# Performance work log

Measured on AMD Instinct MI355X. Metric: run time of the kernel, lower is better.

The kernel has to match this reference:

```python
import jax, jax.numpy as jnp
import numpy as np

B, S, D, H = 2, 2048, 1024, 16
HD = D // H  # head dim = 64

def setup_inputs() -> dict:
    key = jax.random.key(0)
    ks = jax.random.split(key, 3)
    scale = 1.0 / np.sqrt(D)
    return {
        "x": jax.random.normal(ks[0], (B, S, D), jnp.float32),
        "W_attn": jax.random.normal(ks[1], (D, 3 * D), jnp.float32) * scale,
        "b_attn": jnp.zeros((3 * D,), jnp.float32),
        "W_proj": jax.random.normal(ks[2], (D, D), jnp.float32) * scale,
        "b_proj": jnp.zeros((D,), jnp.float32),
    }

def reference(x, W_attn, b_attn, W_proj, b_proj):
    b, s, d = x.shape
    qkv = x @ W_attn + b_attn                      # [B,S,3D]
    q, k, v = jnp.split(qkv, 3, axis=-1)
    # [B,S,D] -> [B,H,S,HD]
    def heads(t):
        return t.reshape(b, s, H, HD).transpose(0, 2, 1, 3)
    q, k, v = heads(q), heads(k), heads(v)
    scores = jnp.einsum('bhqd,bhkd->bhqk', q, k) * (1.0 / np.sqrt(HD))
    causal = jnp.tril(jnp.ones((s, s), dtype=bool))
    scores = jnp.where(causal[None, None], scores, -jnp.inf)
    probs = jax.nn.softmax(scores, axis=-1)
    y = jnp.einsum('bhqk,bhkd->bhqd', probs, v)    # [B,H,S,HD]
    y = y.transpose(0, 2, 1, 3).reshape(b, s, d)
    return y @ W_proj + b_proj
```

## Files before the change

### kernel.cpp

```cpp
#include <hip/hip_runtime.h>

typedef __bf16 bf16;
typedef __bf16 bf16x4 __attribute__((ext_vector_type(4)));
typedef __bf16 bf16x8 __attribute__((ext_vector_type(8)));
typedef float f32x4 __attribute__((ext_vector_type(4)));

#define S_LEN 2048
#define D_DIM 1024
#define N_HEAD 16
#define HEAD_DIM 64
#define M_TOK 4096
#define BH 32

#define EXP2F(x) __builtin_amdgcn_exp2f(x)
#define Q_SCALE 0.18033688f

#define SW(r, c) ((c) ^ (((r) & 3) << 4))

typedef __attribute__((address_space(3))) void lds_void;
typedef const __attribute__((address_space(1))) void gbl_void;

__device__ __forceinline__ void gl_lds16(const bf16* g, bf16* l) {
  __builtin_amdgcn_global_load_lds((gbl_void*)g, (lds_void*)l, 16, 0, 0);
}

__global__ __launch_bounds__(256) void k_cast(const float* __restrict__ x,
                                              bf16* __restrict__ o, int n) {
  int i = (blockIdx.x * 256 + threadIdx.x) * 4;
  if (i >= n) return;
  float4 v = *(const float4*)(x + i);
  bf16x4 w;
  w[0] = (bf16)v.x; w[1] = (bf16)v.y; w[2] = (bf16)v.z; w[3] = (bf16)v.w;
  *(bf16x4*)(o + i) = w;
}

__global__ __launch_bounds__(256) void k_transpose(const float* __restrict__ W,
                                                   bf16* __restrict__ Wt,
                                                   int K, int N) {
  __shared__ float tile[32][33];
  int nb = blockIdx.x, kb = blockIdx.y;
  int t = threadIdx.x;
  int r = t >> 3, c4 = (t & 7) * 4;
  float4 v = *(const float4*)&W[(kb * 32 + r) * N + nb * 32 + c4];
  tile[r][c4 + 0] = v.x; tile[r][c4 + 1] = v.y;
  tile[r][c4 + 2] = v.z; tile[r][c4 + 3] = v.w;
  __syncthreads();
  bf16x4 o;
  #pragma unroll
  for (int i = 0; i < 4; i++) o[i] = (bf16)tile[c4 + i][r];
  *(bf16x4*)&Wt[(nb * 32 + r) * K + kb * 32 + c4] = o;
}

__global__ __launch_bounds__(256, 2)
void k_gemm_qkv(const bf16* __restrict__ A, const bf16* __restrict__ Bt,
                const float* __restrict__ bias,
                bf16* __restrict__ qk, bf16* __restrict__ vT) {
  __shared__ bf16 As[128 * 32];
  __shared__ bf16 Bs[128 * 32];
  const int K = 1024;
  int bn = blockIdx.x, bm = blockIdx.y;
  int t = threadIdx.x;
  int wave = t >> 6, lane = t & 63, c = lane & 15, quad = lane >> 4;
  int wm = wave & 1, wn = wave >> 1;
  int ldrow = lane >> 2, ldcol = (lane & 3) * 8;

  const bf16* Ag = A + (size_t)(bm * 128) * K;
  const bf16* Bg = Bt + (size_t)(bn * 128) * K;

  f32x4 acc[4][4] = {};

  for (int k0 = 0; k0 < K; k0 += 32) {
    __syncthreads();
    #pragma unroll
    for (int q = 0; q < 2; q++) {
      int r0 = (wave * 2 + q) * 16;
      gl_lds16(&Ag[(size_t)(r0 + ldrow) * K + k0 + ldcol], &As[r0 * 32]);
      gl_lds16(&Bg[(size_t)(r0 + ldrow) * K + k0 + ldcol], &Bs[r0 * 32]);
    }
    __syncthreads();
    bf16x8 af[4];
    #pragma unroll
    for (int mt = 0; mt < 4; mt++)
      af[mt] = *(const bf16x8*)&As[(wm * 64 + mt * 16 + c) * 32 + quad * 8];
    #pragma unroll
    for (int nt = 0; nt < 4; nt++) {
      bf16x8 bfr = *(const bf16x8*)&Bs[(wn * 64 + nt * 16 + c) * 32 + quad * 8];
      #pragma unroll
      for (int mt = 0; mt < 4; mt++)
        acc[mt][nt] = __builtin_amdgcn_mfma_f32_16x16x32_bf16(af[mt], bfr, acc[mt][nt], 0, 0, 0);
    }
  }

  #pragma unroll
  for (int nt = 0; nt < 4; nt++) {
    int n = bn * 128 + wn * 64 + nt * 16 + c;
    int which = n >> 10, nl = n & 1023;
    int h = nl >> 6, hd = nl & 63;
    float bv = bias[n];
    #pragma unroll
    for (int mt = 0; mt < 4; mt++) {
      int m0 = bm * 128 + wm * 64 + mt * 16 + quad * 4;
      int b = m0 >> 11, s0 = m0 & 2047;
      int bh = b * N_HEAD + h;
      if (which == 2) {
        bf16x4 o;
        #pragma unroll
        for (int r = 0; r < 4; r++) o[r] = (bf16)(acc[mt][nt][r] + bv);
        *(bf16x4*)&vT[((size_t)bh * HEAD_DIM + hd) * S_LEN + s0] = o;
      } else if (which == 0) {
        #pragma unroll
        for (int r = 0; r < 4; r++)
          qk[(bh * S_LEN + s0 + r) * HEAD_DIM + hd] = (bf16)((acc[mt][nt][r] + bv) * Q_SCALE);
      } else {
        #pragma unroll
        for (int r = 0; r < 4; r++)
          qk[BH * S_LEN * HEAD_DIM + (bh * S_LEN + s0 + r) * HEAD_DIM + hd] = (bf16)(acc[mt][nt][r] + bv);
      }
    }
  }
}

__global__ __launch_bounds__(256, 2)
void k_attn(const bf16* __restrict__ qk, const bf16* __restrict__ vT,
            bf16* __restrict__ y) {
  __shared__ bf16 Ks[2][64][64];
  __shared__ bf16 Vs[2][64][64];
  __shared__ bf16 Ps[128][64];
  int bx = blockIdx.x;
  int bh = bx & 31;
  int p = bx >> 5;
  int t = threadIdx.x, w = t >> 6, lane = t & 63, c = lane & 15, quad = lane >> 4;
  const bf16* Qg = qk + (size_t)bh * (S_LEN * HEAD_DIM);
  const bf16* Kg = qk + (size_t)(BH + bh) * (S_LEN * HEAD_DIM);
  const bf16* Vg = vT + (size_t)bh * (HEAD_DIM * S_LEN);
  int b = bh >> 4, h = bh & 15;
  int srow = t >> 3, scol = (t & 7) * 8;
  int swcol = SW(srow, scol);

  const int tileQ0 = p, tileQ1 = 31 - p;
  const int nkb = 32 - p;
  const int dthr = w * 16 + c;

  bf16x8 qf[2][2];
  f32x4 acc[2][4] = {};
  float mM[2] = {-1e30f, -1e30f}, lL[2] = {0.f, 0.f};
  {
    int qr0 = tileQ0 * 64 + w * 16 + c;
    int qr1 = tileQ1 * 64 + w * 16 + c;
    qf[0][0] = *(const bf16x8*)&Qg[qr0 * HEAD_DIM + quad * 8];
    qf[0][1] = *(const bf16x8*)&Qg[qr0 * HEAD_DIM + 32 + quad * 8];
    qf[1][0] = *(const bf16x8*)&Qg[qr1 * HEAD_DIM + quad * 8];
    qf[1][1] = *(const bf16x8*)&Qg[qr1 * HEAD_DIM + 32 + quad * 8];
  }

  bf16x8 kr0 = *(const bf16x8*)&Kg[srow * HEAD_DIM + scol];
  bf16x8 kr1 = *(const bf16x8*)&Kg[(srow + 32) * HEAD_DIM + scol];
  bf16x8 vr0 = *(const bf16x8*)&Vg[(size_t)srow * S_LEN + scol];
  bf16x8 vr1 = *(const bf16x8*)&Vg[(size_t)(srow + 32) * S_LEN + scol];
  *(bf16x8*)&Ks[0][srow][swcol] = kr0;
  *(bf16x8*)&Ks[0][srow + 32][swcol] = kr1;
  *(bf16x8*)&Vs[0][srow][swcol] = vr0;
  *(bf16x8*)&Vs[0][srow + 32][swcol] = vr1;

  for (int kb = 0; kb < nkb; kb++) {
    __syncthreads();
    int cur = kb & 1;
    bool haveNext = (kb + 1 < nkb);
    if (haveNext) {
      kr0 = *(const bf16x8*)&Kg[((kb + 1) * 64 + srow) * HEAD_DIM + scol];
      kr1 = *(const bf16x8*)&Kg[((kb + 1) * 64 + srow + 32) * HEAD_DIM + scol];
      vr0 = *(const bf16x8*)&Vg[(size_t)srow * S_LEN + (kb + 1) * 64 + scol];
      vr1 = *(const bf16x8*)&Vg[(size_t)(srow + 32) * S_LEN + (kb + 1) * 64 + scol];
    }

    bool act0 = (kb <= p);
    bool dia0 = (kb == p);
    bool dia1 = (kb == 31 - p);

    f32x4 sc[2][4];
    #pragma unroll
    for (int kt = 0; kt < 4; kt++) {
      int kr = kt * 16 + c;
      bf16x8 kf0 = *(const bf16x8*)&Ks[cur][kr][SW(kr, quad * 8)];
      bf16x8 kf1 = *(const bf16x8*)&Ks[cur][kr][SW(kr, 32 + quad * 8)];
      if (act0) {
        f32x4 z = {};
        z = __builtin_amdgcn_mfma_f32_16x16x32_bf16(kf0, qf[0][0], z, 0, 0, 0);
        z = __builtin_amdgcn_mfma_f32_16x16x32_bf16(kf1, qf[0][1], z, 0, 0, 0);
        sc[0][kt] = z;
      }
      f32x4 z = {};
      z = __builtin_amdgcn_mfma_f32_16x16x32_bf16(kf0, qf[1][0], z, 0, 0, 0);
      z = __builtin_amdgcn_mfma_f32_16x16x32_bf16(kf1, qf[1][1], z, 0, 0, 0);
      sc[1][kt] = z;
    }

    if (dia0) {
      #pragma unroll
      for (int kt = 0; kt < 4; kt++)
        #pragma unroll
        for (int r = 0; r < 4; r++)
          if (kt * 16 + quad * 4 + r > dthr) sc[0][kt][r] = -1e30f;
    }
    if (dia1) {
      #pragma unroll
      for (int kt = 0; kt < 4; kt++)
        #pragma unroll
        for (int r = 0; r < 4; r++)
          if (kt * 16 + quad * 4 + r > dthr) sc[1][kt][r] = -1e30f;
    }

    #pragma unroll
    for (int st = 0; st < 2; st++) {
      if (st == 0 && !act0) continue;
      float mx = sc[st][0][0];
      #pragma unroll
      for (int kt = 0; kt < 4; kt++)
        #pragma unroll
        for (int r = 0; r < 4; r++) mx = fmaxf(mx, sc[st][kt][r]);
      mx = fmaxf(mx, __shfl_xor(mx, 16));
      mx = fmaxf(mx, __shfl_xor(mx, 32));
      float mnew = fmaxf(mM[st], mx);
      float alpha = EXP2F(mM[st] - mnew);
      float sum = 0.f;
      int prow = st * 64 + w * 16 + c;
      #pragma unroll
      for (int kt = 0; kt < 4; kt++) {
        bf16x4 pk;
        #pragma unroll
        for (int r = 0; r < 4; r++) {
          float pv = EXP2F(sc[st][kt][r] - mnew);
          sum += pv;
          pk[r] = (bf16)pv;
        }
        *(bf16x4*)&Ps[prow][SW(prow, kt * 16 + quad * 4)] = pk;
      }
      sum += __shfl_xor(sum, 16);
      sum += __shfl_xor(sum, 32);
      lL[st] = lL[st] * alpha + sum;
      mM[st] = mnew;
      #pragma unroll
      for (int dt = 0; dt < 4; dt++)
        #pragma unroll
        for (int r = 0; r < 4; r++) acc[st][dt][r] *= alpha;
    }

    #pragma unroll
    for (int ks = 0; ks < 2; ks++) {
      int prow1 = 64 + w * 16 + c;
      bf16x8 pf1 = *(const bf16x8*)&Ps[prow1][SW(prow1, ks * 32 + quad * 8)];
      bf16x8 pf0;
      if (act0) {
        int prow0 = w * 16 + c;
        pf0 = *(const bf16x8*)&Ps[prow0][SW(prow0, ks * 32 + quad * 8)];
      }
      #pragma unroll
      for (int dt = 0; dt < 4; dt++) {
        int vrow = dt * 16 + c;
        bf16x8 vf = *(const bf16x8*)&Vs[cur][vrow][SW(vrow, ks * 32 + quad * 8)];
        if (act0)
          acc[0][dt] = __builtin_amdgcn_mfma_f32_16x16x32_bf16(vf, pf0, acc[0][dt], 0, 0, 0);
        acc[1][dt] = __builtin_amdgcn_mfma_f32_16x16x32_bf16(vf, pf1, acc[1][dt], 0, 0, 0);
      }
    }

    if (haveNext) {
      int nxt = cur ^ 1;
      *(bf16x8*)&Ks[nxt][srow][swcol] = kr0;
      *(bf16x8*)&Ks[nxt][srow + 32][swcol] = kr1;
      *(bf16x8*)&Vs[nxt][srow][swcol] = vr0;
      *(bf16x8*)&Vs[nxt][srow + 32][swcol] = vr1;
    }
  }

  #pragma unroll
  for (int st = 0; st < 2; st++) {
    int q = (st == 0 ? tileQ0 : tileQ1) * 64 + w * 16 + c;
    float linv = 1.0f / lL[st];
    #pragma unroll
    for (int dt = 0; dt < 4; dt++) {
      bf16x4 o;
      #pragma unroll
      for (int r = 0; r < 4; r++) o[r] = (bf16)(acc[st][dt][r] * linv);
      *(bf16x4*)&y[((size_t)(b * S_LEN + q) * N_HEAD + h) * HEAD_DIM + dt * 16 + quad * 4] = o;
    }
  }
}

__global__ __launch_bounds__(256, 2)
void k_gemm_proj(const bf16* __restrict__ A, const bf16* __restrict__ Bt,
                 const float* __restrict__ bias, float* __restrict__ out) {
  __shared__ bf16 As[128 * 32];
  __shared__ bf16 Bs[64 * 32];
  const int K = 1024;
  int bn = blockIdx.x, bm = blockIdx.y;
  int t = threadIdx.x;
  int wave = t >> 6, lane = t & 63, c = lane & 15, quad = lane >> 4;
  int wm = wave & 1, wn = wave >> 1;
  int ldrow = lane >> 2, ldcol = (lane & 3) * 8;

  const bf16* Ag = A + (size_t)(bm * 128) * K;
  const bf16* Bg = Bt + (size_t)(bn * 64) * K;

  f32x4 acc[4][2] = {};

  for (int k0 = 0; k0 < K; k0 += 32) {
    __syncthreads();
    #pragma unroll
    for (int q = 0; q < 2; q++) {
      int r0 = (wave * 2 + q) * 16;
      gl_lds16(&Ag[(size_t)(r0 + ldrow) * K + k0 + ldcol], &As[r0 * 32]);
    }
    gl_lds16(&Bg[(size_t)(wave * 16 + ldrow) * K + k0 + ldcol], &Bs[wave * 16 * 32]);
    __syncthreads();
    bf16x8 af[4];
    #pragma unroll
    for (int mt = 0; mt < 4; mt++)
      af[mt] = *(const bf16x8*)&As[(wm * 64 + mt * 16 + c) * 32 + quad * 8];
    #pragma unroll
    for (int nt = 0; nt < 2; nt++) {
      bf16x8 bfr = *(const bf16x8*)&Bs[(wn * 32 + nt * 16 + c) * 32 + quad * 8];
      #pragma unroll
      for (int mt = 0; mt < 4; mt++)
        acc[mt][nt] = __builtin_amdgcn_mfma_f32_16x16x32_bf16(af[mt], bfr, acc[mt][nt], 0, 0, 0);
    }
  }

  #pragma unroll
  for (int nt = 0; nt < 2; nt++) {
    int n = bn * 64 + wn * 32 + nt * 16 + c;
    float bv = bias[n];
    #pragma unroll
    for (int mt = 0; mt < 4; mt++) {
      #pragma unroll
      for (int r = 0; r < 4; r++) {
        int m = bm * 128 + wm * 64 + mt * 16 + quad * 4 + r;
        out[(size_t)m * D_DIM + n] = acc[mt][nt][r] + bv;
      }
    }
  }
}

extern "C" void kernel_launch(void* const* d_in, const int* in_sizes, int n_in,
                              void* d_out, int out_size, void* d_ws, size_t ws_size,
                              hipStream_t stream) {
  const float* x      = (const float*)d_in[0];
  const float* W_attn = (const float*)d_in[1];
  const float* b_attn = (const float*)d_in[2];
  const float* W_proj = (const float*)d_in[3];
  const float* b_proj = (const float*)d_in[4];
  float* out = (float*)d_out;

  bf16* x_bf = (bf16*)d_ws;
  bf16* wat  = x_bf + 4096 * 1024;
  bf16* wpt  = wat + 3072 * 1024;
  bf16* qk   = wpt + 1024 * 1024;
  bf16* vT   = qk + 8 * 1024 * 1024;
  bf16* y_bf = vT + 4 * 1024 * 1024;

  k_cast<<<4096, 256, 0, stream>>>(x, x_bf, 4096 * 1024);
  k_transpose<<<dim3(3072 / 32, 1024 / 32), 256, 0, stream>>>(W_attn, wat, 1024, 3072);
  k_transpose<<<dim3(1024 / 32, 1024 / 32), 256, 0, stream>>>(W_proj, wpt, 1024, 1024);
  k_gemm_qkv<<<dim3(24, 32), 256, 0, stream>>>(x_bf, wat, b_attn, qk, vT);
  k_attn<<<512, 256, 0, stream>>>(qk, vT, y_bf);
  k_gemm_proj<<<dim3(16, 32), 256, 0, stream>>>(y_bf, wpt, b_proj, out);
}
```

Measured before the change: 190.7 us.

## Split paired causal Q tiles into one tile per block, heaviest-first ordering

Measured after the change: 186.5 us. 2.2% less time.

```diff
diff --git a/kernel.cpp b/kernel.cpp
--- a/kernel.cpp
+++ b/kernel.cpp
@@ -120,15 +120,15 @@
   }
 }
 
-__global__ __launch_bounds__(256, 2)
+__global__ __launch_bounds__(256, 4)
 void k_attn(const bf16* __restrict__ qk, const bf16* __restrict__ vT,
             bf16* __restrict__ y) {
   __shared__ bf16 Ks[2][64][64];
   __shared__ bf16 Vs[2][64][64];
-  __shared__ bf16 Ps[128][64];
+  __shared__ bf16 Ps[64][64];
   int bx = blockIdx.x;
   int bh = bx & 31;
-  int p = bx >> 5;
+  int tile = 31 - (bx >> 5);
   int t = threadIdx.x, w = t >> 6, lane = t & 63, c = lane & 15, quad = lane >> 4;
   const bf16* Qg = qk + (size_t)bh * (S_LEN * HEAD_DIM);
   const bf16* Kg = qk + (size_t)(BH + bh) * (S_LEN * HEAD_DIM);
@@ -137,20 +137,16 @@
   int srow = t >> 3, scol = (t & 7) * 8;
   int swcol = SW(srow, scol);
 
-  const int tileQ0 = p, tileQ1 = 31 - p;
-  const int nkb = 32 - p;
+  const int nkb = tile + 1;
   const int dthr = w * 16 + c;
 
-  bf16x8 qf[2][2];
-  f32x4 acc[2][4] = {};
-  float mM[2] = {-1e30f, -1e30f}, lL[2] = {0.f, 0.f};
+  bf16x8 qf[2];
+  f32x4 acc[4] = {};
+  float mM = -1e30f, lL = 0.f;
   {
-    int qr0 = tileQ0 * 64 + w * 16 + c;
-    int qr1 = tileQ1 * 64 + w * 16 + c;
-    qf[0][0] = *(const bf16x8*)&Qg[qr0 * HEAD_DIM + quad * 8];
-    qf[0][1] = *(const bf16x8*)&Qg[qr0 * HEAD_DIM + 32 + quad * 8];
-    qf[1][0] = *(const bf16x8*)&Qg[qr1 * HEAD_DIM + quad * 8];
-    qf[1][1] = *(const bf16x8*)&Qg[qr1 * HEAD_DIM + 32 + quad * 8];
+    int qr = tile * 64 + w * 16 + c;
+    qf[0] = *(const bf16x8*)&Qg[qr * HEAD_DIM + quad * 8];
+    qf[1] = *(const bf16x8*)&Qg[qr * HEAD_DIM + 32 + quad * 8];
   }
 
   bf16x8 kr0 = *(const bf16x8*)&Kg[srow * HEAD_DIM + scol];
@@ -173,63 +169,46 @@
       vr1 = *(const bf16x8*)&Vg[(size_t)(srow + 32) * S_LEN + (kb + 1) * 64 + scol];
     }
 
-    bool act0 = (kb <= p);
-    bool dia0 = (kb == p);
-    bool dia1 = (kb == 31 - p);
-
-    f32x4 sc[2][4];
+    bool dia = (kb == tile);
+
+    f32x4 sc[4];
     #pragma unroll
     for (int kt = 0; kt < 4; kt++) {
       int kr = kt * 16 + c;
       bf16x8 kf0 = *(const bf16x8*)&Ks[cur][kr][SW(kr, quad * 8)];
       bf16x8 kf1 = *(const bf16x8*)&Ks[cur][kr][SW(kr, 32 + quad * 8)];
-      if (act0) {
-        f32x4 z = {};
-        z = __builtin_amdgcn_mfma_f32_16x16x32_bf16(kf0, qf[0][0], z, 0, 0, 0);
-        z = __builtin_amdgcn_mfma_f32_16x16x32_bf16(kf1, qf[0][1], z, 0, 0, 0);
-        sc[0][kt] = z;
-      }
       f32x4 z = {};
-      z = __builtin_amdgcn_mfma_f32_16x16x32_bf16(kf0, qf[1][0], z, 0, 0, 0);
-      z = __builtin_amdgcn_mfma_f32_16x16x32_bf16(kf1, qf[1][1], z, 0, 0, 0);
-      sc[1][kt] = z;
-    }
-
-    if (dia0) {
+      z = __builtin_amdgcn_mfma_f32_16x16x32_bf16(kf0, qf[0], z, 0, 0, 0);
+      z = __builtin_amdgcn_mfma_f32_16x16x32_bf16(kf1, qf[1], z, 0, 0, 0);
+      sc[kt] = z;
+    }
+
+    if (dia) {
       #pragma unroll
       for (int kt = 0; kt < 4; kt++)
         #pragma unroll
         for (int r = 0; r < 4; r++)
-          if (kt * 16 + quad * 4 + r > dthr) sc[0][kt][r] = -1e30f;
-    }
-    if (dia1) {
+          if (kt * 16 + quad * 4 + r > dthr) sc[kt][r] = -1e30f;
+    }
+
+    {
+      float mx = sc[0][0];
       #pragma unroll
       for (int kt = 0; kt < 4; kt++)
         #pragma unroll
-        for (int r = 0; r < 4; r++)
-          if (kt * 16 + quad * 4 + r > dthr) sc[1][kt][r] = -1e30f;
-    }
-
-    #pragma unroll
-    for (int st = 0; st < 2; st++) {
-      if (st == 0 && !act0) continue;
-      float mx = sc[st][0][0];
-      #pragma unroll
-      for (int kt = 0; kt < 4; kt++)
-        #pragma unroll
-        for (int r = 0; r < 4; r++) mx = fmaxf(mx, sc[st][kt][r]);
+        for (int r = 0; r < 4; r++) mx = fmaxf(mx, sc[kt][r]);
       mx = fmaxf(mx, __shfl_xor(mx, 16));
       mx = fmaxf(mx, __shfl_xor(mx, 32));
-      float mnew = fmaxf(mM[st], mx);
-      float alpha = EXP2F(mM[st] - mnew);
+      float mnew = fmaxf(mM, mx);
+      float alpha = EXP2F(mM - mnew);
       float sum = 0.f;
-      int prow = st * 64 + w * 16 + c;
+      int prow = w * 16 + c;
       #pragma unroll
       for (int kt = 0; kt < 4; kt++) {
         bf16x4 pk;
         #pragma unroll
         for (int r = 0; r < 4; r++) {
-          float pv = EXP2F(sc[st][kt][r] - mnew);
+          float pv = EXP2F(sc[kt][r] - mnew);
           sum += pv;
           pk[r] = (bf16)pv;
         }
@@ -237,30 +216,25 @@
       }
       sum += __shfl_xor(sum, 16);
       sum += __shfl_xor(sum, 32);
-      lL[st] = lL[st] * alpha + sum;
-      mM[st] = mnew;
+      lL = lL * alpha + sum;
+      mM = mnew;
       #pragma unroll
       for (int dt = 0; dt < 4; dt++)
         #pragma unroll
-        for (int r = 0; r < 4; r++) acc[st][dt][r] *= alpha;
-    }
-
-    #pragma unroll
-    for (int ks = 0; ks < 2; ks++) {
-      int prow1 = 64 + w * 16 + c;
-      bf16x8 pf1 = *(const bf16x8*)&Ps[prow1][SW(prow1, ks * 32 + quad * 8)];
-      bf16x8 pf0;
-      if (act0) {
-        int prow0 = w * 16 + c;
-        pf0 = *(const bf16x8*)&Ps[prow0][SW(prow0, ks * 32 + quad * 8)];
-      }
-      #pragma unroll
-      for (int dt = 0; dt < 4; dt++) {
-        int vrow = dt * 16 + c;
-        bf16x8 vf = *(const bf16x8*)&Vs[cur][vrow][SW(vrow, ks * 32 + quad * 8)];
-        if (act0)
-          acc[0][dt] = __builtin_amdgcn_mfma_f32_16x16x32_bf16(vf, pf0, acc[0][dt], 0, 0, 0);
-        acc[1][dt] = __builtin_amdgcn_mfma_f32_16x16x32_bf16(vf, pf1, acc[1][dt], 0, 0, 0);
+        for (int r = 0; r < 4; r++) acc[dt][r] *= alpha;
+    }
+
+    {
+      int prow = w * 16 + c;
+      #pragma unroll
+      for (int ks = 0; ks < 2; ks++) {
+        bf16x8 pf = *(const bf16x8*)&Ps[prow][SW(prow, ks * 32 + quad * 8)];
+        #pragma unroll
+        for (int dt = 0; dt < 4; dt++) {
+          int vrow = dt * 16 + c;
+          bf16x8 vf = *(const bf16x8*)&Vs[cur][vrow][SW(vrow, ks * 32 + quad * 8)];
+          acc[dt] = __builtin_amdgcn_mfma_f32_16x16x32_bf16(vf, pf, acc[dt], 0, 0, 0);
+        }
       }
     }
 
@@ -273,15 +247,14 @@
     }
   }
 
-  #pragma unroll
-  for (int st = 0; st < 2; st++) {
-    int q = (st == 0 ? tileQ0 : tileQ1) * 64 + w * 16 + c;
-    float linv = 1.0f / lL[st];
+  {
+    int q = tile * 64 + w * 16 + c;
+    float linv = 1.0f / lL;
     #pragma unroll
     for (int dt = 0; dt < 4; dt++) {
       bf16x4 o;
       #pragma unroll
-      for (int r = 0; r < 4; r++) o[r] = (bf16)(acc[st][dt][r] * linv);
+      for (int r = 0; r < 4; r++) o[r] = (bf16)(acc[dt][r] * linv);
       *(bf16x4*)&y[((size_t)(b * S_LEN + q) * N_HEAD + h) * HEAD_DIM + dt * 16 + quad * 4] = o;
     }
   }
@@ -362,6 +335,6 @@
   k_transpose<<<dim3(3072 / 32, 1024 / 32), 256, 0, stream>>>(W_attn, wat, 1024, 3072);
   k_transpose<<<dim3(1024 / 32, 1024 / 32), 256, 0, stream>>>(W_proj, wpt, 1024, 1024);
   k_gemm_qkv<<<dim3(24, 32), 256, 0, stream>>>(x_bf, wat, b_attn, qk, vT);
-  k_attn<<<512, 256, 0, stream>>>(qk, vT, y_bf);
+  k_attn<<<1024, 256, 0, stream>>>(qk, vT, y_bf);
   k_gemm_proj<<<dim3(16, 32), 256, 0, stream>>>(y_bf, wpt, b_proj, out);
 }
```
